# Optimization experiments

Measured on AMD Instinct MI355X. Metric: run time of the kernel, lower is better.

Reference implementation:

```python
import jax, jax.numpy as jnp
import numpy as np

B, C, H, W = 8, 192, 128, 128
WS, SHIFT, NH = 8, 4, 6
HD = C // NH
HID = 4 * C
N = WS * WS


def _rel_pos_index(ws):
    coords = np.stack(np.meshgrid(np.arange(ws), np.arange(ws), indexing='ij')).reshape(2, -1)
    rel = coords[:, :, None] - coords[:, None, :]
    rel = rel.transpose(1, 2, 0).copy()
    rel[:, :, 0] += ws - 1
    rel[:, :, 1] += ws - 1
    rel[:, :, 0] *= 2 * ws - 1
    return rel.sum(-1)  # (ws*ws, ws*ws) int

REL_IDX = _rel_pos_index(WS)


def setup_inputs() -> dict:
    key = jax.random.key(0)
    ks = jax.random.split(key, 8)
    s = 0.02
    return {
        'x': jax.random.normal(ks[0], (B, C, H, W), jnp.float32),
        'g1': jnp.ones((C,), jnp.float32), 'b1': jnp.zeros((C,), jnp.float32),
        'qkv_w': (jax.random.normal(ks[1], (C, 3 * C), jnp.float32) * s),
        'qkv_b': jnp.zeros((3 * C,), jnp.float32),
        'proj_w': (jax.random.normal(ks[2], (C, C), jnp.float32) * s),
        'proj_b': jnp.zeros((C,), jnp.float32),
        'rpb': (jax.random.normal(ks[3], ((2 * WS - 1) ** 2, NH), jnp.float32) * s),
        'g2': jnp.ones((C,), jnp.float32), 'b2': jnp.zeros((C,), jnp.float32),
        'fc1_w': (jax.random.normal(ks[4], (C, HID), jnp.float32) * s),
        'fc1_b': jnp.zeros((HID,), jnp.float32),
        'fc2_w': (jax.random.normal(ks[5], (HID, C), jnp.float32) * s),
        'fc2_b': jnp.zeros((C,), jnp.float32),
    }


def _ln(t, g, b):
    m = t.mean(-1, keepdims=True)
    v = t.var(-1, keepdims=True)
    return (t - m) / jnp.sqrt(v + 1e-5) * g + b


def reference(x, g1, b1, qkv_w, qkv_b, proj_w, proj_b, rpb, g2, b2, fc1_w, fc1_b, fc2_w, fc2_b):
    shortcut = x                                  # (B,C,H,W)
    xl = x.transpose(0, 2, 3, 1)                  # (B,H,W,C)
    xn = _ln(xl, g1, b1)
    xs = jnp.roll(xn, (-SHIFT, -SHIFT), axis=(1, 2))
    # window partition -> (B*nw, N, C)
    xw = xs.reshape(B, H // WS, WS, W // WS, WS, C).transpose(0, 1, 3, 2, 4, 5).reshape(-1, N, C)
    qkv = (xw @ qkv_w + qkv_b).reshape(-1, N, 3, NH, HD).transpose(2, 0, 3, 1, 4)
    q, k, v = qkv[0] * (HD ** -0.5), qkv[1], qkv[2]   # (B_, NH, N, HD)
    attn = jnp.einsum('bhnd,bhmd->bhnm', q, k)
    bias = rpb[REL_IDX.reshape(-1)].reshape(N, N, NH).transpose(2, 0, 1)  # (NH,N,N)
    attn = jax.nn.softmax(attn + bias[None], axis=-1)
    out = jnp.einsum('bhnm,bhmd->bnhd', attn, v).reshape(-1, N, C)
    out = out @ proj_w + proj_b
    # window reverse -> (B,H,W,C)
    out = out.reshape(B, H // WS, W // WS, WS, WS, C).transpose(0, 1, 3, 2, 4, 5).reshape(B, H, W, C)
    out = jnp.roll(out, (SHIFT, SHIFT), axis=(1, 2))
    x2 = shortcut + out.transpose(0, 3, 1, 2)     # (B,C,H,W)
    xn2 = _ln(x2.transpose(0, 2, 3, 1), g2, b2)   # (B,H,W,C)
    h = jax.nn.gelu(xn2 @ fc1_w + fc1_b, approximate=False)
    mlp = (h @ fc2_w + fc2_b).transpose(0, 3, 1, 2)
    return x2 + mlp
```

## Files before the change

### kernel.cpp

```cpp
#include <hip/hip_runtime.h>
#include <hip/hip_bf16.h>
#include <math.h>

typedef __bf16 bf16;
typedef __bf16 bf16x8 __attribute__((ext_vector_type(8)));
typedef float f32x4 __attribute__((ext_vector_type(4)));

__device__ __forceinline__ f32x4 mfma16(bf16x8 a, bf16x8 b, f32x4 c) {
    return __builtin_amdgcn_mfma_f32_16x16x32_bf16(a, b, c, 0, 0, 0);
}

constexpr int Bv = 8, Cc = 192, Hh = 128, Wd = 128;
constexpr int HW = Hh * Wd;
constexpr int NWIN = 2048;

constexpr size_t OFF_XW    = 0;
constexpr size_t SZ_XW     = (size_t)NWIN * 64 * 192 * 2;
constexpr size_t OFF_QKVWT = SZ_XW;
constexpr size_t OFF_PROJT = OFF_QKVWT + 576 * 192 * 2;
constexpr size_t OFF_FC1T  = OFF_PROJT + 192 * 192 * 2;
constexpr size_t OFF_FC2T  = OFF_FC1T + 768 * 192 * 2;

__global__ void wconv_kernel(const float* __restrict__ qkv_w, const float* __restrict__ proj_w,
                             const float* __restrict__ fc1_w, const float* __restrict__ fc2_w,
                             bf16* __restrict__ qkvT, bf16* __restrict__ projT,
                             bf16* __restrict__ fc1T, bf16* __restrict__ fc2T) {
    int bid = blockIdx.x;
    const float* src; bf16* dst; int K, Nw, base;
    if (bid < 432)       { src = qkv_w;  dst = qkvT;  K = 192; Nw = 576; base = bid; }
    else if (bid < 576)  { src = proj_w; dst = projT; K = 192; Nw = 192; base = bid - 432; }
    else if (bid < 1152) { src = fc1_w;  dst = fc1T;  K = 192; Nw = 768; base = bid - 576; }
    else                 { src = fc2_w;  dst = fc2T;  K = 768; Nw = 192; base = bid - 1152; }
    int idx = base * 256 + threadIdx.x;
    if (idx < K * Nw) {
        int n = idx / K, k = idx % K;
        dst[idx] = (bf16)src[k * Nw + n];
    }
}

__global__ void __launch_bounds__(256) ln1win_kernel(const float* __restrict__ x,
                                                     const float* __restrict__ g1,
                                                     const float* __restrict__ b1,
                                                     bf16* __restrict__ xw) {
    __shared__ float xT[192][65];
    __shared__ float part[2][4][64];
    __shared__ float mrs[2][64];
    int win = blockIdx.x;
    int b = win >> 8, wi = (win >> 4) & 15, wj = win & 15;
    int tid = threadIdx.x, wave = tid >> 6, t = tid & 63;
    int p = t >> 3, q = t & 7;
    int h = (wi * 8 + p + 4) & 127, w = (wj * 8 + q + 4) & 127;
    const float* xp = x + (size_t)b * 192 * HW + h * 128 + w;
    float sum = 0.f, ssq = 0.f;
    for (int i = 0; i < 48; i++) {
        int c = wave * 48 + i;
        float v = xp[(size_t)c * HW];
        xT[c][t] = v; sum += v; ssq += v * v;
    }
    part[0][wave][t] = sum; part[1][wave][t] = ssq;
    __syncthreads();
    if (tid < 64) {
        float s = 0.f, s2 = 0.f;
        for (int ww = 0; ww < 4; ww++) { s += part[0][ww][tid]; s2 += part[1][ww][tid]; }
        float mean = s * (1.f / 192.f);
        float var = s2 * (1.f / 192.f) - mean * mean;
        mrs[0][tid] = mean; mrs[1][tid] = rsqrtf(var + 1e-5f);
    }
    __syncthreads();
    bf16* op = xw + (size_t)win * 64 * 192;
    for (int it = 0; it < 48; it++) {
        int e = it * 256 + tid;
        int n = e / 192, c = e % 192;
        float v = (xT[c][n] - mrs[0][n]) * mrs[1][n] * g1[c] + b1[c];
        op[e] = (bf16)v;
    }
}

__global__ void __launch_bounds__(256, 2) attn_kernel(const float* __restrict__ x,
                                                      const bf16* __restrict__ xw,
                                                      const bf16* __restrict__ qkvT,
                                                      const float* __restrict__ qkv_b,
                                                      const bf16* __restrict__ projT,
                                                      const float* __restrict__ proj_b,
                                                      const float* __restrict__ rpb,
                                                      float* __restrict__ out) {
    __shared__ __align__(16) char smem[66816];
    bf16*  q_lds  = (bf16*)(smem);
    bf16*  k_lds  = (bf16*)(smem + 5120);
    bf16*  vT_lds = (bf16*)(smem + 10240);
    float* s_lds  = (float*)(smem + 14848);
    bf16*  p_lds  = (bf16*)(smem + 32000);
    bf16*  ao_lds = (bf16*)(smem + 41216);
    bf16*  mo_lds = (bf16*)(smem);

    int win = blockIdx.x;
    int b = win >> 8, wi = (win >> 4) & 15, wj = win & 15;
    int tid = threadIdx.x;
    int wv = tid >> 6, l = tid & 63, lo = l & 15, hi = l >> 4;
    int m0 = wv * 16;

    const bf16x8* xwp = (const bf16x8*)(xw + (size_t)win * 64 * 192);
    bf16x8 afr[6];
#pragma unroll
    for (int kt = 0; kt < 6; kt++) afr[kt] = xwp[(m0 + lo) * 24 + kt * 4 + hi];

    const bf16x8* qkvw8 = (const bf16x8*)qkvT;
    for (int hd = 0; hd < 6; hd++) {
#pragma unroll
        for (int cg = 0; cg < 6; cg++) {
            int part = cg >> 1, ctl = cg & 1;
            int brow = part * 192 + hd * 32 + ctl * 16 + lo;
            f32x4 acc = {0.f, 0.f, 0.f, 0.f};
#pragma unroll
            for (int kt = 0; kt < 6; kt++)
                acc = mfma16(afr[kt], qkvw8[brow * 24 + kt * 4 + hi], acc);
            float bias = qkv_b[brow];
            if (part == 0) {
#pragma unroll
                for (int r = 0; r < 4; r++)
                    q_lds[(m0 + hi * 4 + r) * 40 + ctl * 16 + lo] =
                        (bf16)((acc[r] + bias) * 0.17677669529663687f);
            } else if (part == 1) {
#pragma unroll
                for (int r = 0; r < 4; r++)
                    k_lds[(m0 + hi * 4 + r) * 40 + ctl * 16 + lo] = (bf16)(acc[r] + bias);
            } else {
#pragma unroll
                for (int r = 0; r < 4; r++)
                    vT_lds[(ctl * 16 + lo) * 72 + (m0 + hi * 4 + r)] = (bf16)(acc[r] + bias);
            }
        }
        __syncthreads();
        {
            bf16x8 a2 = *(const bf16x8*)&q_lds[(m0 + lo) * 40 + hi * 8];
#pragma unroll
            for (int ct = 0; ct < 4; ct++) {
                bf16x8 b2 = *(const bf16x8*)&k_lds[(ct * 16 + lo) * 40 + hi * 8];
                f32x4 sc = {0.f, 0.f, 0.f, 0.f};
                sc = mfma16(a2, b2, sc);
                int mk = ct * 16 + lo, i2 = mk >> 3, j2 = mk & 7;
#pragma unroll
                for (int r = 0; r < 4; r++) {
                    int nq = m0 + hi * 4 + r, i1 = nq >> 3, j1 = nq & 7;
                    int ridx = (i1 - i2 + 7) * 15 + (j1 - j2 + 7);
                    s_lds[nq * 67 + mk] = sc[r] + rpb[ridx * 6 + hd];
                }
            }
        }
        __syncthreads();
        {
            int row = tid >> 2, seg = tid & 3;
            const float* sr = &s_lds[row * 67 + seg * 16];
            float ev[16];
            float mx = -1e30f;
#pragma unroll
            for (int j = 0; j < 16; j++) { ev[j] = sr[j]; mx = fmaxf(mx, ev[j]); }
            mx = fmaxf(mx, __shfl_xor(mx, 1));
            mx = fmaxf(mx, __shfl_xor(mx, 2));
            float sum = 0.f;
#pragma unroll
            for (int j = 0; j < 16; j++) { ev[j] = __expf(ev[j] - mx); sum += ev[j]; }
            sum += __shfl_xor(sum, 1);
            sum += __shfl_xor(sum, 2);
            float inv = 1.f / sum;
            bf16* pr = &p_lds[row * 72 + seg * 16];
#pragma unroll
            for (int j = 0; j < 16; j++) pr[j] = (bf16)(ev[j] * inv);
        }
        __syncthreads();
#pragma unroll
        for (int ct = 0; ct < 2; ct++) {
            f32x4 acc = {0.f, 0.f, 0.f, 0.f};
#pragma unroll
            for (int kt = 0; kt < 2; kt++) {
                bf16x8 a3 = *(const bf16x8*)&p_lds[(m0 + lo) * 72 + kt * 32 + hi * 8];
                bf16x8 b3 = *(const bf16x8*)&vT_lds[(ct * 16 + lo) * 72 + kt * 32 + hi * 8];
                acc = mfma16(a3, b3, acc);
            }
#pragma unroll
            for (int r = 0; r < 4; r++)
                ao_lds[(m0 + hi * 4 + r) * 200 + hd * 32 + ct * 16 + lo] = (bf16)acc[r];
        }
        __syncthreads();
    }
    bf16x8 a4[6];
#pragma unroll
    for (int kt = 0; kt < 6; kt++)
        a4[kt] = *(const bf16x8*)&ao_lds[(m0 + lo) * 200 + kt * 32 + hi * 8];
    const bf16x8* pw8 = (const bf16x8*)projT;
#pragma unroll
    for (int ct = 0; ct < 12; ct++) {
        int cc = ct * 16 + lo;
        f32x4 acc = {0.f, 0.f, 0.f, 0.f};
#pragma unroll
        for (int kt = 0; kt < 6; kt++)
            acc = mfma16(a4[kt], pw8[cc * 24 + kt * 4 + hi], acc);
        float pb = proj_b[cc];
#pragma unroll
        for (int r = 0; r < 4; r++)
            mo_lds[cc * 68 + m0 + hi * 4 + r] = (bf16)(acc[r] + pb);
    }
    __syncthreads();
    size_t obase = (size_t)b * 192 * HW;
    for (int it = 0; it < 48; it++) {
        int e = it * 256 + tid;
        int c = e >> 6, t = e & 63;
        int hh = (wi * 8 + (t >> 3) + 4) & 127;
        int ww2 = (wj * 8 + (t & 7) + 4) & 127;
        size_t addr = obase + (size_t)c * HW + hh * 128 + ww2;
        out[addr] = x[addr] + (float)mo_lds[c * 68 + t];
    }
}

__global__ void __launch_bounds__(256, 2) mlp_kernel(const float* __restrict__ g2,
                                                     const float* __restrict__ b2,
                                                     const bf16* __restrict__ fc1T,
                                                     const float* __restrict__ fc1_b,
                                                     const bf16* __restrict__ fc2T,
                                                     const float* __restrict__ fc2_b,
                                                     float* __restrict__ out) {
    __shared__ __align__(16) char smem[75776];
    bf16*  xn2  = (bf16*)smem;
    bf16*  hbuf = (bf16*)(smem + 25600);
    float* part = (float*)(smem + 25600);
    float* mrs  = (float*)(smem + 25600 + 2048);
    bf16*  mo   = (bf16*)smem;

    int pix0 = blockIdx.x * 64;
    int b = pix0 >> 14, rem = pix0 & 16383;
    int hh = rem >> 7, w0 = rem & 127;
    int tid = threadIdx.x, wv = tid >> 6, t = tid & 63;
    int lo = t & 15, hi = t >> 4;
    float* xrow = out + (size_t)b * 192 * HW + hh * 128 + w0;

    float sum = 0.f, ssq = 0.f;
    for (int i = 0; i < 48; i++) {
        int c = wv * 48 + i;
        float v = xrow[(size_t)c * HW + t];
        sum += v; ssq += v * v;
    }
    part[(0 * 4 + wv) * 64 + t] = sum; part[(1 * 4 + wv) * 64 + t] = ssq;
    __syncthreads();
    if (tid < 64) {
        float s = 0.f, s2 = 0.f;
        for (int ww = 0; ww < 4; ww++) { s += part[ww * 64 + tid]; s2 += part[(4 + ww) * 64 + tid]; }
        float mean = s * (1.f / 192.f);
        float var = s2 * (1.f / 192.f) - mean * mean;
        mrs[tid] = mean; mrs[64 + tid] = rsqrtf(var + 1e-5f);
    }
    __syncthreads();
    for (int i = 0; i < 48; i++) {
        int c = wv * 48 + i;
        float v = xrow[(size_t)c * HW + t];
        xn2[t * 200 + c] = (bf16)((v - mrs[t]) * mrs[64 + t] * g2[c] + b2[c]);
    }
    __syncthreads();

    bf16x8 axn[4][6];
#pragma unroll
    for (int mt = 0; mt < 4; mt++)
#pragma unroll
        for (int kt = 0; kt < 6; kt++)
            axn[mt][kt] = *(const bf16x8*)&xn2[(mt * 16 + lo) * 200 + kt * 32 + hi * 8];

    f32x4 oacc[3][4];
#pragma unroll
    for (int ct = 0; ct < 3; ct++)
#pragma unroll
        for (int mt = 0; mt < 4; mt++) oacc[ct][mt] = {0.f, 0.f, 0.f, 0.f};

    const bf16x8* f1 = (const bf16x8*)fc1T;
    const bf16x8* f2 = (const bf16x8*)fc2T;

    for (int hf = 0; hf < 2; hf++) {
#pragma unroll
        for (int ct = 0; ct < 6; ct++) {
            int nb = hf * 384 + wv * 96 + ct * 16 + lo;
            f32x4 acc[4];
#pragma unroll
            for (int mt = 0; mt < 4; mt++) acc[mt] = {0.f, 0.f, 0.f, 0.f};
#pragma unroll
            for (int kt = 0; kt < 6; kt++) {
                bf16x8 bfr = f1[nb * 24 + kt * 4 + hi];
#pragma unroll
                for (int mt = 0; mt < 4; mt++)
                    acc[mt] = mfma16(axn[mt][kt], bfr, acc[mt]);
            }
            float bb = fc1_b[nb];
            int col = wv * 96 + ct * 16 + lo;
#pragma unroll
            for (int mt = 0; mt < 4; mt++)
#pragma unroll
                for (int r = 0; r < 4; r++) {
                    float y = acc[mt][r] + bb;
                    float g = 0.5f * y * (1.f + erff(y * 0.70710678118f));
                    hbuf[(mt * 16 + hi * 4 + r) * 392 + col] = (bf16)g;
                }
        }
        __syncthreads();
#pragma unroll
        for (int kt = 0; kt < 12; kt++) {
            bf16x8 afr[4];
#pragma unroll
            for (int mt = 0; mt < 4; mt++)
                afr[mt] = *(const bf16x8*)&hbuf[(mt * 16 + lo) * 392 + kt * 32 + hi * 8];
            bf16x8 bfr[3];
#pragma unroll
            for (int ct = 0; ct < 3; ct++) {
                int cc = wv * 48 + ct * 16 + lo;
                bfr[ct] = f2[cc * 96 + hf * 48 + kt * 4 + hi];
            }
#pragma unroll
            for (int ct = 0; ct < 3; ct++)
#pragma unroll
                for (int mt = 0; mt < 4; mt++)
                    oacc[ct][mt] = mfma16(afr[mt], bfr[ct], oacc[ct][mt]);
        }
        __syncthreads();
    }

#pragma unroll
    for (int ct = 0; ct < 3; ct++) {
        int cc = wv * 48 + ct * 16 + lo;
        float fb = fc2_b[cc];
#pragma unroll
        for (int mt = 0; mt < 4; mt++)
#pragma unroll
            for (int r = 0; r < 4; r++)
                mo[cc * 68 + mt * 16 + hi * 4 + r] = (bf16)(oacc[ct][mt][r] + fb);
    }
    __syncthreads();
    for (int it = 0; it < 48; it++) {
        int e = it * 256 + tid;
        int c = e >> 6, t2 = e & 63;
        size_t a = (size_t)c * HW + t2;
        xrow[a] = xrow[a] + (float)mo[c * 68 + t2];
    }
}

extern "C" void kernel_launch(void* const* d_in, const int* in_sizes, int n_in,
                              void* d_out, int out_size, void* d_ws, size_t ws_size,
                              hipStream_t stream) {
    const float* x      = (const float*)d_in[0];
    const float* g1     = (const float*)d_in[1];
    const float* b1     = (const float*)d_in[2];
    const float* qkv_w  = (const float*)d_in[3];
    const float* qkv_b  = (const float*)d_in[4];
    const float* proj_w = (const float*)d_in[5];
    const float* proj_b = (const float*)d_in[6];
    const float* rpb    = (const float*)d_in[7];
    const float* g2     = (const float*)d_in[8];
    const float* b2     = (const float*)d_in[9];
    const float* fc1_w  = (const float*)d_in[10];
    const float* fc1_b  = (const float*)d_in[11];
    const float* fc2_w  = (const float*)d_in[12];
    const float* fc2_b  = (const float*)d_in[13];
    float* out = (float*)d_out;
    char* ws = (char*)d_ws;
    bf16* xw    = (bf16*)(ws + OFF_XW);
    bf16* qkvT  = (bf16*)(ws + OFF_QKVWT);
    bf16* projT = (bf16*)(ws + OFF_PROJT);
    bf16* fc1T  = (bf16*)(ws + OFF_FC1T);
    bf16* fc2T  = (bf16*)(ws + OFF_FC2T);

    wconv_kernel<<<1728, 256, 0, stream>>>(qkv_w, proj_w, fc1_w, fc2_w, qkvT, projT, fc1T, fc2T);
    ln1win_kernel<<<2048, 256, 0, stream>>>(x, g1, b1, xw);
    attn_kernel<<<2048, 256, 0, stream>>>(x, xw, qkvT, qkv_b, projT, proj_b, rpb, out);
    mlp_kernel<<<2048, 256, 0, stream>>>(g2, b2, fc1T, fc1_b, fc2T, fc2_b, out);
}
```

Baseline: 826.4 us.

## Shrink LDS and registers in attention and MLP kernels for three blocks per CU

The attention kernel now folds the output projection into the per-head loop, accumulating into register accumulators. This removes the full attention-output LDS buffer, and the padding strides are retuned. The MLP kernel splits the hidden dimension into four quarters instead of two and uses XOR-swizzled unpadded LDS layouts. It also reloads the LayerNorm A-fragments from LDS each step instead of holding them in registers. Together these cut shared memory to about 51 KB and raise launch bounds to three blocks per CU, trading extra LDS/global reloads and more barriers for higher occupancy.

```diff
diff --git a/kernel.cpp b/kernel.cpp
--- a/kernel.cpp
+++ b/kernel.cpp
@@ -10,7 +10,7 @@
     return __builtin_amdgcn_mfma_f32_16x16x32_bf16(a, b, c, 0, 0, 0);
 }
 
-constexpr int Bv = 8, Cc = 192, Hh = 128, Wd = 128;
+constexpr int Hh = 128, Wd = 128;
 constexpr int HW = Hh * Wd;
 constexpr int NWIN = 2048;
 
@@ -76,7 +76,7 @@
     }
 }
 
-__global__ void __launch_bounds__(256, 2) attn_kernel(const float* __restrict__ x,
+__global__ void __launch_bounds__(256, 3) attn_kernel(const float* __restrict__ x,
                                                       const bf16* __restrict__ xw,
                                                       const bf16* __restrict__ qkvT,
                                                       const float* __restrict__ qkv_b,
@@ -84,13 +84,13 @@
                                                       const float* __restrict__ proj_b,
                                                       const float* __restrict__ rpb,
                                                       float* __restrict__ out) {
-    __shared__ __align__(16) char smem[66816];
+    __shared__ __align__(16) char smem[51712];
     bf16*  q_lds  = (bf16*)(smem);
     bf16*  k_lds  = (bf16*)(smem + 5120);
     bf16*  vT_lds = (bf16*)(smem + 10240);
-    float* s_lds  = (float*)(smem + 14848);
-    bf16*  p_lds  = (bf16*)(smem + 32000);
-    bf16*  ao_lds = (bf16*)(smem + 41216);
+    float* s_lds  = (float*)(smem + 15872);
+    bf16*  p_lds  = (bf16*)(smem + 35328);
+    bf16*  po_lds = (bf16*)(smem + 46592);
     bf16*  mo_lds = (bf16*)(smem);
 
     int win = blockIdx.x;
@@ -99,13 +99,18 @@
     int wv = tid >> 6, l = tid & 63, lo = l & 15, hi = l >> 4;
     int m0 = wv * 16;
 
-    const bf16x8* xwp = (const bf16x8*)(xw + (size_t)win * 64 * 192);
-    bf16x8 afr[6];
-#pragma unroll
-    for (int kt = 0; kt < 6; kt++) afr[kt] = xwp[(m0 + lo) * 24 + kt * 4 + hi];
-
+    const bf16x8* xwp   = (const bf16x8*)(xw + (size_t)win * 64 * 192);
     const bf16x8* qkvw8 = (const bf16x8*)qkvT;
+    const bf16x8* pw8   = (const bf16x8*)projT;
+
+    f32x4 projacc[12];
+#pragma unroll
+    for (int i = 0; i < 12; i++) projacc[i] = {0.f, 0.f, 0.f, 0.f};
+
     for (int hd = 0; hd < 6; hd++) {
+        bf16x8 afr[6];
+#pragma unroll
+        for (int kt = 0; kt < 6; kt++) afr[kt] = xwp[(m0 + lo) * 24 + kt * 4 + hi];
 #pragma unroll
         for (int cg = 0; cg < 6; cg++) {
             int part = cg >> 1, ctl = cg & 1;
@@ -127,7 +132,7 @@
             } else {
 #pragma unroll
                 for (int r = 0; r < 4; r++)
-                    vT_lds[(ctl * 16 + lo) * 72 + (m0 + hi * 4 + r)] = (bf16)(acc[r] + bias);
+                    vT_lds[(ctl * 16 + lo) * 88 + (m0 + hi * 4 + r)] = (bf16)(acc[r] + bias);
             }
         }
         __syncthreads();
@@ -143,14 +148,14 @@
                 for (int r = 0; r < 4; r++) {
                     int nq = m0 + hi * 4 + r, i1 = nq >> 3, j1 = nq & 7;
                     int ridx = (i1 - i2 + 7) * 15 + (j1 - j2 + 7);
-                    s_lds[nq * 67 + mk] = sc[r] + rpb[ridx * 6 + hd];
+                    s_lds[nq * 76 + mk] = sc[r] + rpb[ridx * 6 + hd];
                 }
             }
         }
         __syncthreads();
         {
             int row = tid >> 2, seg = tid & 3;
-            const float* sr = &s_lds[row * 67 + seg * 16];
+            const float* sr = &s_lds[row * 76 + seg * 16];
             float ev[16];
             float mx = -1e30f;
 #pragma unroll
@@ -163,7 +168,7 @@
             sum += __shfl_xor(sum, 1);
             sum += __shfl_xor(sum, 2);
             float inv = 1.f / sum;
-            bf16* pr = &p_lds[row * 72 + seg * 16];
+            bf16* pr = &p_lds[row * 88 + seg * 16];
 #pragma unroll
             for (int j = 0; j < 16; j++) pr[j] = (bf16)(ev[j] * inv);
         }
@@ -173,32 +178,32 @@
             f32x4 acc = {0.f, 0.f, 0.f, 0.f};
 #pragma unroll
             for (int kt = 0; kt < 2; kt++) {
-                bf16x8 a3 = *(const bf16x8*)&p_lds[(m0 + lo) * 72 + kt * 32 + hi * 8];
-                bf16x8 b3 = *(const bf16x8*)&vT_lds[(ct * 16 + lo) * 72 + kt * 32 + hi * 8];
+                bf16x8 a3 = *(const bf16x8*)&p_lds[(m0 + lo) * 88 + kt * 32 + hi * 8];
+                bf16x8 b3 = *(const bf16x8*)&vT_lds[(ct * 16 + lo) * 88 + kt * 32 + hi * 8];
                 acc = mfma16(a3, b3, acc);
             }
 #pragma unroll
             for (int r = 0; r < 4; r++)
-                ao_lds[(m0 + hi * 4 + r) * 200 + hd * 32 + ct * 16 + lo] = (bf16)acc[r];
-        }
-        __syncthreads();
-    }
-    bf16x8 a4[6];
-#pragma unroll
-    for (int kt = 0; kt < 6; kt++)
-        a4[kt] = *(const bf16x8*)&ao_lds[(m0 + lo) * 200 + kt * 32 + hi * 8];
-    const bf16x8* pw8 = (const bf16x8*)projT;
-#pragma unroll
-    for (int ct = 0; ct < 12; ct++) {
-        int cc = ct * 16 + lo;
-        f32x4 acc = {0.f, 0.f, 0.f, 0.f};
-#pragma unroll
-        for (int kt = 0; kt < 6; kt++)
-            acc = mfma16(a4[kt], pw8[cc * 24 + kt * 4 + hi], acc);
+                po_lds[(m0 + hi * 4 + r) * 40 + ct * 16 + lo] = (bf16)acc[r];
+        }
+        __syncthreads();
+        {
+            bf16x8 a4 = *(const bf16x8*)&po_lds[(m0 + lo) * 40 + hi * 8];
+#pragma unroll
+            for (int ct2 = 0; ct2 < 12; ct2++) {
+                bf16x8 bf = pw8[(ct2 * 16 + lo) * 24 + hd * 4 + hi];
+                projacc[ct2] = mfma16(a4, bf, projacc[ct2]);
+            }
+        }
+    }
+    __syncthreads();
+#pragma unroll
+    for (int ct2 = 0; ct2 < 12; ct2++) {
+        int cc = ct2 * 16 + lo;
         float pb = proj_b[cc];
 #pragma unroll
         for (int r = 0; r < 4; r++)
-            mo_lds[cc * 68 + m0 + hi * 4 + r] = (bf16)(acc[r] + pb);
+            mo_lds[cc * 68 + m0 + hi * 4 + r] = (bf16)(projacc[ct2][r] + pb);
     }
     __syncthreads();
     size_t obase = (size_t)b * 192 * HW;
@@ -212,18 +217,18 @@
     }
 }
 
-__global__ void __launch_bounds__(256, 2) mlp_kernel(const float* __restrict__ g2,
+__global__ void __launch_bounds__(256, 3) mlp_kernel(const float* __restrict__ g2,
                                                      const float* __restrict__ b2,
                                                      const bf16* __restrict__ fc1T,
                                                      const float* __restrict__ fc1_b,
                                                      const bf16* __restrict__ fc2T,
                                                      const float* __restrict__ fc2_b,
                                                      float* __restrict__ out) {
-    __shared__ __align__(16) char smem[75776];
+    __shared__ __align__(16) char smem[51712];
     bf16*  xn2  = (bf16*)smem;
-    bf16*  hbuf = (bf16*)(smem + 25600);
-    float* part = (float*)(smem + 25600);
-    float* mrs  = (float*)(smem + 25600 + 2048);
+    bf16*  hbuf = (bf16*)(smem + 24576);
+    float* part = (float*)(smem + 49152);
+    float* mrs  = (float*)(smem + 51200);
     bf16*  mo   = (bf16*)smem;
 
     int pix0 = blockIdx.x * 64;
@@ -239,7 +244,7 @@
         float v = xrow[(size_t)c * HW + t];
         sum += v; ssq += v * v;
     }
-    part[(0 * 4 + wv) * 64 + t] = sum; part[(1 * 4 + wv) * 64 + t] = ssq;
+    part[wv * 64 + t] = sum; part[(4 + wv) * 64 + t] = ssq;
     __syncthreads();
     if (tid < 64) {
         float s = 0.f, s2 = 0.f;
@@ -252,16 +257,10 @@
     for (int i = 0; i < 48; i++) {
         int c = wv * 48 + i;
         float v = xrow[(size_t)c * HW + t];
-        xn2[t * 200 + c] = (bf16)((v - mrs[t]) * mrs[64 + t] * g2[c] + b2[c]);
-    }
-    __syncthreads();
-
-    bf16x8 axn[4][6];
-#pragma unroll
-    for (int mt = 0; mt < 4; mt++)
-#pragma unroll
-        for (int kt = 0; kt < 6; kt++)
-            axn[mt][kt] = *(const bf16x8*)&xn2[(mt * 16 + lo) * 200 + kt * 32 + hi * 8];
+        int g = (c >> 3) ^ (t & 7);
+        xn2[t * 192 + g * 8 + (c & 7)] = (bf16)((v - mrs[t]) * mrs[64 + t] * g2[c] + b2[c]);
+    }
+    __syncthreads();
 
     f32x4 oacc[3][4];
 #pragma unroll
@@ -272,49 +271,64 @@
     const bf16x8* f1 = (const bf16x8*)fc1T;
     const bf16x8* f2 = (const bf16x8*)fc2T;
 
-    for (int hf = 0; hf < 2; hf++) {
-#pragma unroll
-        for (int ct = 0; ct < 6; ct++) {
-            int nb = hf * 384 + wv * 96 + ct * 16 + lo;
-            f32x4 acc[4];
-#pragma unroll
-            for (int mt = 0; mt < 4; mt++) acc[mt] = {0.f, 0.f, 0.f, 0.f};
-#pragma unroll
-            for (int kt = 0; kt < 6; kt++) {
+    for (int qd = 0; qd < 4; qd++) {
+        f32x4 acc[3][4];
+#pragma unroll
+        for (int ct = 0; ct < 3; ct++)
+#pragma unroll
+            for (int mt = 0; mt < 4; mt++) acc[ct][mt] = {0.f, 0.f, 0.f, 0.f};
+#pragma unroll
+        for (int kt = 0; kt < 6; kt++) {
+            bf16x8 a[4];
+#pragma unroll
+            for (int mt = 0; mt < 4; mt++) {
+                int row = mt * 16 + lo;
+                int g = (kt * 4 + hi) ^ (row & 7);
+                a[mt] = *(const bf16x8*)&xn2[row * 192 + g * 8];
+            }
+#pragma unroll
+            for (int ct = 0; ct < 3; ct++) {
+                int nb = qd * 192 + wv * 48 + ct * 16 + lo;
                 bf16x8 bfr = f1[nb * 24 + kt * 4 + hi];
 #pragma unroll
                 for (int mt = 0; mt < 4; mt++)
-                    acc[mt] = mfma16(axn[mt][kt], bfr, acc[mt]);
-            }
+                    acc[ct][mt] = mfma16(a[mt], bfr, acc[ct][mt]);
+            }
+        }
+#pragma unroll
+        for (int ct = 0; ct < 3; ct++) {
+            int nb = qd * 192 + wv * 48 + ct * 16 + lo;
             float bb = fc1_b[nb];
-            int col = wv * 96 + ct * 16 + lo;
+            int hcol = wv * 48 + ct * 16 + lo;
 #pragma unroll
             for (int mt = 0; mt < 4; mt++)
 #pragma unroll
                 for (int r = 0; r < 4; r++) {
-                    float y = acc[mt][r] + bb;
+                    float y = acc[ct][mt][r] + bb;
                     float g = 0.5f * y * (1.f + erff(y * 0.70710678118f));
-                    hbuf[(mt * 16 + hi * 4 + r) * 392 + col] = (bf16)g;
+                    int row = mt * 16 + hi * 4 + r;
+                    int gg = (hcol >> 3) ^ (row & 7);
+                    hbuf[row * 192 + gg * 8 + (hcol & 7)] = (bf16)g;
                 }
         }
         __syncthreads();
 #pragma unroll
-        for (int kt = 0; kt < 12; kt++) {
-            bf16x8 afr[4];
-#pragma unroll
-            for (int mt = 0; mt < 4; mt++)
-                afr[mt] = *(const bf16x8*)&hbuf[(mt * 16 + lo) * 392 + kt * 32 + hi * 8];
-            bf16x8 bfr[3];
+        for (int kt = 0; kt < 6; kt++) {
+            bf16x8 ah[4];
+#pragma unroll
+            for (int mt = 0; mt < 4; mt++) {
+                int row = mt * 16 + lo;
+                int g = (kt * 4 + hi) ^ (row & 7);
+                ah[mt] = *(const bf16x8*)&hbuf[row * 192 + g * 8];
+            }
 #pragma unroll
             for (int ct = 0; ct < 3; ct++) {
                 int cc = wv * 48 + ct * 16 + lo;
-                bfr[ct] = f2[cc * 96 + hf * 48 + kt * 4 + hi];
-            }
-#pragma unroll
-            for (int ct = 0; ct < 3; ct++)
+                bf16x8 bfr = f2[cc * 96 + qd * 24 + kt * 4 + hi];
 #pragma unroll
                 for (int mt = 0; mt < 4; mt++)
-                    oacc[ct][mt] = mfma16(afr[mt], bfr[ct], oacc[ct][mt]);
+                    oacc[ct][mt] = mfma16(ah[mt], bfr, oacc[ct][mt]);
+            }
         }
         __syncthreads();
     }
```

Result: slower. 968.1 us (+17.1%).
